# Kernel tuning notes

Hardware: AMD Instinct MI355X
Metric: run time of the kernel (lower is better)

The kernel has to match this reference:

```python
import jax, jax.numpy as jnp
import numpy as np

N_NODES = 50000
N_EDGES = 800000
N_FEAT = 128
HIDDEN = 128
N_CLASSES = 10
N_GRAPHS = 100


def setup_inputs() -> dict:
    key = jax.random.key(0)
    ks = jax.random.split(key, 16)
    x = jax.random.normal(ks[0], (N_NODES, N_FEAT), dtype=jnp.float32)
    edge_index = jax.random.randint(ks[1], (2, N_EDGES), 0, N_NODES, dtype=jnp.int64)
    batch = jnp.sort(jax.random.randint(ks[2], (N_NODES,), 0, N_GRAPHS, dtype=jnp.int64))

    def glorot(k, fi, fo):
        s = jnp.sqrt(6.0 / (fi + fo)).astype(jnp.float32)
        return jax.random.uniform(k, (fi, fo), jnp.float32, -s, s)

    return {
        "x": x,
        "edge_index": edge_index,
        "batch": batch,
        "W1": glorot(ks[3], N_FEAT, HIDDEN),
        "b1": jnp.zeros((HIDDEN,), jnp.float32),
        "W2": glorot(ks[4], HIDDEN, HIDDEN),
        "b2": jnp.zeros((HIDDEN,), jnp.float32),
        "W3": glorot(ks[5], HIDDEN, HIDDEN // 2),
        "b3": jnp.zeros((HIDDEN // 2,), jnp.float32),
        "Wf1": glorot(ks[6], HIDDEN // 2, 32),
        "bf1": jnp.zeros((32,), jnp.float32),
        "Wf2": glorot(ks[7], 32, N_CLASSES),
        "bf2": jnp.zeros((N_CLASSES,), jnp.float32),
    }


def _gcn_conv(x, row, col, norm, W, b, n_nodes):
    # GCNConv: x' = D^{-1/2}(A+I)D^{-1/2} (x W) + b
    h = x @ W                                            # [N, out]
    msg = h[row] * norm[:, None]                         # gather + scale per edge
    out = jax.ops.segment_sum(msg, col, num_segments=n_nodes)  # scatter-add to targets
    return out + b


def reference(x, edge_index, batch, W1, b1, W2, b2, W3, b3, Wf1, bf1, Wf2, bf2):
    n = x.shape[0]
    # add self-loops (PyG GCNConv default)
    loop = jnp.arange(n, dtype=edge_index.dtype)
    row = jnp.concatenate([edge_index[0], loop])
    col = jnp.concatenate([edge_index[1], loop])
    # symmetric normalization from in-degree at targets (edge_weight = 1)
    deg = jax.ops.segment_sum(jnp.ones_like(col, x.dtype), col, num_segments=n)
    dinv = jnp.where(deg > 0, jax.lax.rsqrt(deg), 0.0)
    norm = dinv[row] * dinv[col]                         # [E + N]

    h = jax.nn.relu(_gcn_conv(x, row, col, norm, W1, b1, n))
    h = jax.nn.relu(_gcn_conv(h, row, col, norm, W2, b2, n))
    h = jax.nn.relu(_gcn_conv(h, row, col, norm, W3, b3, n))

    # global_mean_pool over graphs
    sums = jax.ops.segment_sum(h, batch, num_segments=N_GRAPHS)
    cnts = jax.ops.segment_sum(jnp.ones((n,), h.dtype), batch, num_segments=N_GRAPHS)
    pooled = sums / jnp.maximum(cnts, 1.0)[:, None]      # [G, hidden//2]

    h = jax.nn.relu(pooled @ Wf1 + bf1)
    logits = h @ Wf2 + bf2                               # [G, num_classes]
    return logits
```

## Files before the change

### kernel.cpp

```cpp
#include <hip/hip_runtime.h>
#include <hip/hip_fp16.h>


#define NGRAPH 100
#define CAP 64

typedef _Float16 f16x8 __attribute__((ext_vector_type(8)));
typedef float f32x4 __attribute__((ext_vector_type(4)));
typedef float fx2 __attribute__((ext_vector_type(2)));
typedef float fx4 __attribute__((ext_vector_type(4)));


__global__ __launch_bounds__(256) void prep_all(const float* __restrict__ W1,
                                                const float* __restrict__ W2,
                                                const float* __restrict__ W3,
                                                __half* __restrict__ Wt1,
                                                __half* __restrict__ Wt2,
                                                __half* __restrict__ Wt3,
                                                int* __restrict__ cnt,
                                                float* __restrict__ pooled, int n) {
    const int idx = blockIdx.x * 256 + threadIdx.x;
    if (idx < 16384) {
        int nn = idx >> 7, k = idx & 127;
        Wt1[idx] = __float2half(W1[k * 128 + nn]);
    } else if (idx < 32768) {
        int j = idx - 16384;
        int nn = j >> 7, k = j & 127;
        Wt2[j] = __float2half(W2[k * 128 + nn]);
    } else if (idx < 40960) {
        int j = idx - 32768;
        int nn = j >> 7, k = j & 127;
        Wt3[j] = __float2half(W3[k * 64 + nn]);
    }
    if (idx < n) cnt[idx] = 0;
    if (idx < NGRAPH * 64) pooled[idx] = 0.0f;
}


__global__ void fill_bucket(const int* __restrict__ row, const int* __restrict__ col,
                            int* __restrict__ cnt, int* __restrict__ bucket,
                            int E, int colsPerGroup) {
    const int g  = blockIdx.x & 7;
    const int gb = blockIdx.x >> 3;
    const int nb = gridDim.x >> 3;
    const int lo = g * colsPerGroup, hi = lo + colsPerGroup;
    for (int e = gb * 256 + threadIdx.x; e < E; e += nb * 256) {
        int c = col[e];
        if (c >= lo && c < hi) {
            int pos = atomicAdd(&cnt[c], 1);
            bucket[c * CAP + pos] = row[e];
        }
    }
}


template <int OUT, bool F16IN>
__global__ __launch_bounds__(256) void gemm_mfma(const void* __restrict__ Xv,
                                                 const __half* __restrict__ Wt,
                                                 const float* __restrict__ bias_in,
                                                 const int* __restrict__ cnt,
                                                 __half* __restrict__ Yh, int n) {
    __shared__ _Float16 Xs[64 * 128];
    __shared__ _Float16 Ws[OUT * 128];
    __shared__ float bs[128];

    const float*  Xf = (const float*)Xv;
    const __half* Xh = (const __half*)Xv;

    const int t = threadIdx.x;
    if (t < 128) bs[t] = (bias_in != nullptr) ? bias_in[t] : 0.0f;
    __syncthreads();

    const int row0 = blockIdx.x * 64;
    const bool do_relu = (bias_in != nullptr);

    for (int c = t; c < 64 * 16; c += 256) {
        const int r = c >> 4, q = c & 15;
        const int gr = row0 + r;
        float vals[8];
        #pragma unroll
        for (int i = 0; i < 8; ++i) vals[i] = 0.0f;
        if (gr < n) {
            if (F16IN) {
                f16x8 hv = *(const f16x8*)&Xh[(size_t)gr * 128 + q * 8];
                #pragma unroll
                for (int i = 0; i < 8; ++i) vals[i] = (float)hv[i];
            } else {
                float4 va = *(const float4*)&Xf[(size_t)gr * 128 + q * 8];
                float4 vb = *(const float4*)&Xf[(size_t)gr * 128 + q * 8 + 4];
                vals[0] = va.x; vals[1] = va.y; vals[2] = va.z; vals[3] = va.w;
                vals[4] = vb.x; vals[5] = vb.y; vals[6] = vb.z; vals[7] = vb.w;
            }
        }
        if (do_relu) {
            const int k = q * 8;
            #pragma unroll
            for (int i = 0; i < 8; ++i) vals[i] = fmaxf(vals[i] + bs[k + i], 0.f);
        }
        f16x8 hv;
        #pragma unroll
        for (int i = 0; i < 8; ++i) hv[i] = (_Float16)vals[i];
        *(f16x8*)&Xs[(size_t)((r << 4) + (q ^ (r & 15))) * 8] = hv;
    }
    for (int c = t; c < OUT * 16; c += 256) {
        const int nn = c >> 4, q = c & 15;
        f16x8 w = *(const f16x8*)&Wt[nn * 128 + q * 8];
        *(f16x8*)&Ws[(size_t)((nn << 4) + (q ^ (nn & 15))) * 8] = w;
    }
    __syncthreads();

    constexpr int NT = OUT / 16;
    const int lane = t & 63, wave = t >> 6;
    const int m = lane & 15, quad = lane >> 4;

    f32x4 acc[NT];
    #pragma unroll
    for (int i = 0; i < NT; ++i) acc[i] = (f32x4){0.f, 0.f, 0.f, 0.f};

    #pragma unroll
    for (int s = 0; s < 4; ++s) {
        const int qa = s * 4 + quad;
        f16x8 a = *(const f16x8*)&Xs[(size_t)(((wave * 16 + m) << 4) + (qa ^ m)) * 8];
        #pragma unroll
        for (int tt = 0; tt < NT; ++tt) {
            f16x8 b = *(const f16x8*)&Ws[(size_t)(((tt * 16 + m) << 4) + (qa ^ m)) * 8];
            acc[tt] = __builtin_amdgcn_mfma_f32_16x16x32_f16(a, b, acc[tt], 0, 0, 0);
        }
    }

    #pragma unroll
    for (int i = 0; i < 4; ++i) {
        const int gr = row0 + wave * 16 + quad * 4 + i;
        if (gr < n) {
            const float dw = 1.0f / sqrtf((float)(cnt[gr] + 1));
            #pragma unroll
            for (int tt = 0; tt < NT; ++tt)
                Yh[(size_t)gr * OUT + tt * 16 + m] = __float2half(acc[tt][i] * dw);
        }
    }
}


template <int F>
__global__ void gather_kernel(const __half* __restrict__ hs, const int* __restrict__ cnt,
                              const int* __restrict__ bucket,
                              __half* __restrict__ outh, int n) {
    const int lane = threadIdx.x & 63;
    const int c = (blockIdx.x * blockDim.x + threadIdx.x) >> 6;
    if (c >= n) return;
    const int deg = cnt[c];
    const int beg = c * CAP;
    const int end = beg + deg;
    const int last = end - 1;
    const float w = 1.0f / sqrtf((float)(deg + 1));
    const float4* hq = (const float4*)hs;

    const int strm = lane >> 4;
    const int li   = lane & 15;

    float a[8];
    #pragma unroll
    for (int i = 0; i < 8; ++i) a[i] = 0.f;

    auto acc8 = [&](float4 raw, float m) {
        __half2 h0 = *(__half2*)&raw.x;
        __half2 h1 = *(__half2*)&raw.y;
        __half2 h2 = *(__half2*)&raw.z;
        __half2 h3 = *(__half2*)&raw.w;
        float2 f0 = __half22float2(h0), f1 = __half22float2(h1);
        float2 f2 = __half22float2(h2), f3 = __half22float2(h3);
        a[0] += m * f0.x; a[1] += m * f0.y;
        a[2] += m * f1.x; a[3] += m * f1.y;
        a[4] += m * f2.x; a[5] += m * f2.y;
        a[6] += m * f3.x; a[7] += m * f3.y;
    };

    if (strm == 0) acc8(hq[(size_t)c * 16 + li], 1.f);

    const int chunks = (deg + 15) >> 4;
    int j = beg + strm;
    for (int t = 0; t < chunks; ++t, j += 16) {
        const int j0 = j, j1 = j + 4, j2 = j + 8, j3 = j + 12;
        const int s0 = __builtin_nontemporal_load(&bucket[min(j0, last)]);
        const int s1 = __builtin_nontemporal_load(&bucket[min(j1, last)]);
        const int s2 = __builtin_nontemporal_load(&bucket[min(j2, last)]);
        const int s3 = __builtin_nontemporal_load(&bucket[min(j3, last)]);
        const float m0 = (j0 < end) ? 1.f : 0.f;
        const float m1 = (j1 < end) ? 1.f : 0.f;
        const float m2 = (j2 < end) ? 1.f : 0.f;
        const float m3 = (j3 < end) ? 1.f : 0.f;
        float4 v0 = hq[(size_t)s0 * 16 + li];
        float4 v1 = hq[(size_t)s1 * 16 + li];
        float4 v2 = hq[(size_t)s2 * 16 + li];
        float4 v3 = hq[(size_t)s3 * 16 + li];
        acc8(v0, m0);
        acc8(v1, m1);
        acc8(v2, m2);
        acc8(v3, m3);
    }

    #pragma unroll
    for (int i = 0; i < 8; ++i) {
        a[i] += __shfl(a[i], lane ^ 16);
        a[i] += __shfl(a[i], lane ^ 32);
    }
    if (strm == 0) {
        __half2 o0 = __float22half2_rn(make_float2(w * a[0], w * a[1]));
        __half2 o1 = __float22half2_rn(make_float2(w * a[2], w * a[3]));
        __half2 o2 = __float22half2_rn(make_float2(w * a[4], w * a[5]));
        __half2 o3 = __float22half2_rn(make_float2(w * a[6], w * a[7]));
        fx4 o;
        o[0] = *(float*)&o0;
        o[1] = *(float*)&o1;
        o[2] = *(float*)&o2;
        o[3] = *(float*)&o3;
        __builtin_nontemporal_store(o, (fx4*)&outh[(size_t)c * 128 + li * 8]);
    }
}


__global__ __launch_bounds__(256) void fused_gpool(const __half* __restrict__ hs,
                                                   const int* __restrict__ cnt,
                                                   const int* __restrict__ bucket,
                                                   const float* __restrict__ b3,
                                                   const int* __restrict__ batch,
                                                   float* __restrict__ pooled, int n) {
    const int lane  = threadIdx.x & 63;
    const int half  = lane >> 5;
    const int li    = lane & 31;
    const int wave  = (blockIdx.x * blockDim.x + threadIdx.x) >> 6;
    const int nwav  = (gridDim.x * blockDim.x) >> 6;
    const int chunk = (n + nwav - 1) / nwav;
    const int beg = wave * chunk;
    const int end = min(beg + chunk, n);
    if (beg >= end) return;
    const unsigned* h2 = (const unsigned*)hs;

    auto cvt2 = [](unsigned raw) { return __half22float2(*(__half2*)&raw); };

    const float bias0 = b3[li * 2], bias1 = b3[li * 2 + 1];
    int curg = batch[beg];
    float2 acc = make_float2(0.f, 0.f);
    for (int i = beg; i < end; ++i) {
        int g = batch[i];
        if (g != curg) {
            if (half == 0) {
                atomicAdd(&pooled[curg * 64 + li * 2],     acc.x);
                atomicAdd(&pooled[curg * 64 + li * 2 + 1], acc.y);
            }
            acc = make_float2(0.f, 0.f); curg = g;
        }
        const int deg = cnt[i];
        const float dv = 1.0f / sqrtf((float)(deg + 1));
        float2 sv = make_float2(0.f, 0.f);
        if (half == 0) sv = cvt2(h2[(size_t)i * 32 + li]);
        const int eb = i * CAP, ee = eb + deg;
        const int lastj = ee - 1;
        const int chks = (deg + 15) >> 4;
        int j = eb + half;
        for (int t = 0; t < chks; ++t, j += 16) {
            const int j0 = j,      j1 = j + 2,  j2 = j + 4,  j3 = j + 6;
            const int j4 = j + 8,  j5 = j + 10, j6 = j + 12, j7 = j + 14;
            const int a0 = __builtin_nontemporal_load(&bucket[min(j0, lastj)]);
            const int a1 = __builtin_nontemporal_load(&bucket[min(j1, lastj)]);
            const int a2 = __builtin_nontemporal_load(&bucket[min(j2, lastj)]);
            const int a3 = __builtin_nontemporal_load(&bucket[min(j3, lastj)]);
            const int a4 = __builtin_nontemporal_load(&bucket[min(j4, lastj)]);
            const int a5 = __builtin_nontemporal_load(&bucket[min(j5, lastj)]);
            const int a6 = __builtin_nontemporal_load(&bucket[min(j6, lastj)]);
            const int a7 = __builtin_nontemporal_load(&bucket[min(j7, lastj)]);
            const float m0 = (j0 < ee) ? 1.f : 0.f;
            const float m1 = (j1 < ee) ? 1.f : 0.f;
            const float m2 = (j2 < ee) ? 1.f : 0.f;
            const float m3 = (j3 < ee) ? 1.f : 0.f;
            const float m4 = (j4 < ee) ? 1.f : 0.f;
            const float m5 = (j5 < ee) ? 1.f : 0.f;
            const float m6 = (j6 < ee) ? 1.f : 0.f;
            const float m7 = (j7 < ee) ? 1.f : 0.f;
            float2 v0 = cvt2(h2[(size_t)a0 * 32 + li]);
            float2 v1 = cvt2(h2[(size_t)a1 * 32 + li]);
            float2 v2 = cvt2(h2[(size_t)a2 * 32 + li]);
            float2 v3 = cvt2(h2[(size_t)a3 * 32 + li]);
            float2 v4 = cvt2(h2[(size_t)a4 * 32 + li]);
            float2 v5 = cvt2(h2[(size_t)a5 * 32 + li]);
            float2 v6 = cvt2(h2[(size_t)a6 * 32 + li]);
            float2 v7 = cvt2(h2[(size_t)a7 * 32 + li]);
            sv.x += m0 * v0.x + m1 * v1.x + m2 * v2.x + m3 * v3.x
                  + m4 * v4.x + m5 * v5.x + m6 * v6.x + m7 * v7.x;
            sv.y += m0 * v0.y + m1 * v1.y + m2 * v2.y + m3 * v3.y
                  + m4 * v4.y + m5 * v5.y + m6 * v6.y + m7 * v7.y;
        }
        sv.x += __shfl(sv.x, lane ^ 32);
        sv.y += __shfl(sv.y, lane ^ 32);
        acc.x += fmaxf(dv * sv.x + bias0, 0.f);
        acc.y += fmaxf(dv * sv.y + bias1, 0.f);
    }
    if (half == 0) {
        atomicAdd(&pooled[curg * 64 + li * 2],     acc.x);
        atomicAdd(&pooled[curg * 64 + li * 2 + 1], acc.y);
    }
}


__global__ __launch_bounds__(64) void mlp_kernel(const float* __restrict__ pooled,
                                                 const int* __restrict__ batch,
                                                 const float* __restrict__ Wf1,
                                                 const float* __restrict__ bf1,
                                                 const float* __restrict__ Wf2,
                                                 const float* __restrict__ bf2,
                                                 float* __restrict__ out, int n) {
    const int g = blockIdx.x;
    const int t = threadIdx.x;

    auto lb = [&](int v) {
        int lo = 0, hi = n;
        while (lo < hi) { int mid = (lo + hi) >> 1; if (batch[mid] < v) lo = mid + 1; else hi = mid; }
        return lo;
    };
    const int cnt = lb(g + 1) - lb(g);

    __shared__ float pm[64];
    __shared__ float hid[32];

    pm[t] = pooled[g * 64 + t] / (float)(cnt > 0 ? cnt : 1);
    __syncthreads();

    if (t < 32) {
        float a = bf1[t];
        #pragma unroll
        for (int k = 0; k < 64; ++k) a += pm[k] * Wf1[k * 32 + t];
        hid[t] = fmaxf(a, 0.f);
    }
    __syncthreads();

    if (t < 10) {
        float a = bf2[t];
        #pragma unroll
        for (int k = 0; k < 32; ++k) a += hid[k] * Wf2[k * 10 + t];
        out[g * 10 + t] = a;
    }
}


extern "C" void kernel_launch(void* const* d_in, const int* in_sizes, int n_in,
                              void* d_out, int out_size, void* d_ws, size_t ws_size,
                              hipStream_t stream) {
    const float* x     = (const float*)d_in[0];
    const int*   edge  = (const int*)  d_in[1];
    const int*   batch = (const int*)  d_in[2];
    const float* W1    = (const float*)d_in[3];
    const float* b1    = (const float*)d_in[4];
    const float* W2    = (const float*)d_in[5];
    const float* b2    = (const float*)d_in[6];
    const float* W3    = (const float*)d_in[7];
    const float* b3    = (const float*)d_in[8];
    const float* Wf1   = (const float*)d_in[9];
    const float* bf1   = (const float*)d_in[10];
    const float* Wf2   = (const float*)d_in[11];
    const float* bf2   = (const float*)d_in[12];
    float* out = (float*)d_out;

    const int E = in_sizes[1] / 2;
    const int n = in_sizes[2];
    const int* row = edge;
    const int* col = edge + E;

    const int colsPerGroup = (n + 7) / 8;

    const size_t n_pad = ((size_t)n + 64) & ~(size_t)63;
    char* wsb = (char*)d_ws;
    int*    cnt    = (int*)wsb;                  wsb += n_pad * 4;
    float*  pooled = (float*)wsb;                wsb += NGRAPH * 64 * 4;
    int*    bucket = (int*)wsb;                  wsb += (size_t)n_pad * CAP * 4;
    __half* Wt1    = (__half*)wsb;               wsb += 16384 * 2;
    __half* Wt2    = (__half*)wsb;               wsb += 16384 * 2;
    __half* Wt3    = (__half*)wsb;               wsb += 8192 * 2;
    __half* bufA   = (__half*)wsb;               wsb += (size_t)n * 128 * 2;
    __half* bufB   = (__half*)wsb;

    prep_all<<<256, 256, 0, stream>>>(W1, W2, W3, Wt1, Wt2, Wt3, cnt, pooled, n);
    fill_bucket<<<1024, 256, 0, stream>>>(row, col, cnt, bucket, E, colsPerGroup);

    const int ggemm = (n + 63) / 64;
    const int gath_grid = (n * 64 + 255) / 256;

    gemm_mfma<128, false><<<ggemm, 256, 0, stream>>>(x, Wt1, nullptr, cnt, bufA, n);
    gather_kernel<128><<<gath_grid, 256, 0, stream>>>(bufA, cnt, bucket, bufB, n);
    gemm_mfma<128, true><<<ggemm, 256, 0, stream>>>(bufB, Wt2, b1, cnt, bufA, n);
    gather_kernel<128><<<gath_grid, 256, 0, stream>>>(bufA, cnt, bucket, bufB, n);
    gemm_mfma<64, true><<<ggemm, 256, 0, stream>>>(bufB, Wt3, b2, cnt, bufA, n);
    fused_gpool<<<2048, 256, 0, stream>>>(bufA, cnt, bucket, b3, batch, pooled, n);
    mlp_kernel<<<NGRAPH, 64, 0, stream>>>(pooled, batch, Wf1, bf1, Wf2, bf2, out, n);
}
```

Baseline: 263.5 us.

## Fuse neighbor gather with following layer GEMM via shared-memory tile

Replaces the separate gather kernel plus GEMM kernel for layers 2 and 3 with one kernel. Each block gathers and aggregates 64 destination rows, applies bias and ReLU, and stores the fp16 result in shared memory. It then runs the MFMA GEMM on that tile directly. This removes the intermediate global write and read of the aggregated features and one launch per layer. The cost is fewer waves in flight during the latency-bound gather phase: 782 blocks, each wave handling 16 rows in sequence, instead of one wave per row.

```diff
diff --git a/kernel.cpp b/kernel.cpp
--- a/kernel.cpp
+++ b/kernel.cpp
@@ -7,8 +7,6 @@
 
 typedef _Float16 f16x8 __attribute__((ext_vector_type(8)));
 typedef float f32x4 __attribute__((ext_vector_type(4)));
-typedef float fx2 __attribute__((ext_vector_type(2)));
-typedef float fx4 __attribute__((ext_vector_type(4)));
 
 
 __global__ __launch_bounds__(256) void prep_all(const float* __restrict__ W1,
@@ -141,80 +139,126 @@
 }
 
 
-template <int F>
-__global__ void gather_kernel(const __half* __restrict__ hs, const int* __restrict__ cnt,
-                              const int* __restrict__ bucket,
-                              __half* __restrict__ outh, int n) {
-    const int lane = threadIdx.x & 63;
-    const int c = (blockIdx.x * blockDim.x + threadIdx.x) >> 6;
-    if (c >= n) return;
-    const int deg = cnt[c];
-    const int beg = c * CAP;
-    const int end = beg + deg;
-    const int last = end - 1;
-    const float w = 1.0f / sqrtf((float)(deg + 1));
-    const float4* hq = (const float4*)hs;
-
+template <int OUT>
+__global__ __launch_bounds__(256) void gather_gemm(const __half* __restrict__ hs,
+                                                   const __half* __restrict__ Wt,
+                                                   const float* __restrict__ bias_in,
+                                                   const int* __restrict__ cnt,
+                                                   const int* __restrict__ bucket,
+                                                   __half* __restrict__ Yh, int n) {
+    __shared__ _Float16 Xs[64 * 128];
+    __shared__ _Float16 Ws[OUT * 128];
+    __shared__ float bs[128];
+
+    const int t = threadIdx.x;
+    if (t < 128) bs[t] = bias_in[t];
+
+    for (int c = t; c < OUT * 16; c += 256) {
+        const int nn = c >> 4, q = c & 15;
+        f16x8 w = *(const f16x8*)&Wt[nn * 128 + q * 8];
+        *(f16x8*)&Ws[(size_t)((nn << 4) + (q ^ (nn & 15))) * 8] = w;
+    }
+    __syncthreads();
+
+    const int row0 = blockIdx.x * 64;
+    const int wave = t >> 6, lane = t & 63;
     const int strm = lane >> 4;
     const int li   = lane & 15;
-
-    float a[8];
-    #pragma unroll
-    for (int i = 0; i < 8; ++i) a[i] = 0.f;
-
-    auto acc8 = [&](float4 raw, float m) {
-        __half2 h0 = *(__half2*)&raw.x;
-        __half2 h1 = *(__half2*)&raw.y;
-        __half2 h2 = *(__half2*)&raw.z;
-        __half2 h3 = *(__half2*)&raw.w;
-        float2 f0 = __half22float2(h0), f1 = __half22float2(h1);
-        float2 f2 = __half22float2(h2), f3 = __half22float2(h3);
-        a[0] += m * f0.x; a[1] += m * f0.y;
-        a[2] += m * f1.x; a[3] += m * f1.y;
-        a[4] += m * f2.x; a[5] += m * f2.y;
-        a[6] += m * f3.x; a[7] += m * f3.y;
-    };
-
-    if (strm == 0) acc8(hq[(size_t)c * 16 + li], 1.f);
-
-    const int chunks = (deg + 15) >> 4;
-    int j = beg + strm;
-    for (int t = 0; t < chunks; ++t, j += 16) {
-        const int j0 = j, j1 = j + 4, j2 = j + 8, j3 = j + 12;
-        const int s0 = __builtin_nontemporal_load(&bucket[min(j0, last)]);
-        const int s1 = __builtin_nontemporal_load(&bucket[min(j1, last)]);
-        const int s2 = __builtin_nontemporal_load(&bucket[min(j2, last)]);
-        const int s3 = __builtin_nontemporal_load(&bucket[min(j3, last)]);
-        const float m0 = (j0 < end) ? 1.f : 0.f;
-        const float m1 = (j1 < end) ? 1.f : 0.f;
-        const float m2 = (j2 < end) ? 1.f : 0.f;
-        const float m3 = (j3 < end) ? 1.f : 0.f;
-        float4 v0 = hq[(size_t)s0 * 16 + li];
-        float4 v1 = hq[(size_t)s1 * 16 + li];
-        float4 v2 = hq[(size_t)s2 * 16 + li];
-        float4 v3 = hq[(size_t)s3 * 16 + li];
-        acc8(v0, m0);
-        acc8(v1, m1);
-        acc8(v2, m2);
-        acc8(v3, m3);
-    }
-
-    #pragma unroll
-    for (int i = 0; i < 8; ++i) {
-        a[i] += __shfl(a[i], lane ^ 16);
-        a[i] += __shfl(a[i], lane ^ 32);
-    }
-    if (strm == 0) {
-        __half2 o0 = __float22half2_rn(make_float2(w * a[0], w * a[1]));
-        __half2 o1 = __float22half2_rn(make_float2(w * a[2], w * a[3]));
-        __half2 o2 = __float22half2_rn(make_float2(w * a[4], w * a[5]));
-        __half2 o3 = __float22half2_rn(make_float2(w * a[6], w * a[7]));
-        fx4 o;
-        o[0] = *(float*)&o0;
-        o[1] = *(float*)&o1;
-        o[2] = *(float*)&o2;
-        o[3] = *(float*)&o3;
-        __builtin_nontemporal_store(o, (fx4*)&outh[(size_t)c * 128 + li * 8]);
+    const float4* hq = (const float4*)hs;
+
+    for (int i = 0; i < 16; ++i) {
+        const int r = wave * 16 + i;
+        const int c = row0 + r;
+        float a[8];
+        #pragma unroll
+        for (int k = 0; k < 8; ++k) a[k] = 0.f;
+
+        auto acc8 = [&](float4 raw, float m) {
+            __half2 h0 = *(__half2*)&raw.x;
+            __half2 h1 = *(__half2*)&raw.y;
+            __half2 h2 = *(__half2*)&raw.z;
+            __half2 h3 = *(__half2*)&raw.w;
+            float2 f0 = __half22float2(h0), f1 = __half22float2(h1);
+            float2 f2 = __half22float2(h2), f3 = __half22float2(h3);
+            a[0] += m * f0.x; a[1] += m * f0.y;
+            a[2] += m * f1.x; a[3] += m * f1.y;
+            a[4] += m * f2.x; a[5] += m * f2.y;
+            a[6] += m * f3.x; a[7] += m * f3.y;
+        };
+
+        int deg = 0;
+        if (c < n) {
+            deg = cnt[c];
+            const int beg = c * CAP;
+            const int end = beg + deg;
+            const int last = end - 1;
+            if (strm == 0) acc8(hq[(size_t)c * 16 + li], 1.f);
+            const int chunks = (deg + 15) >> 4;
+            int j = beg + strm;
+            for (int tt = 0; tt < chunks; ++tt, j += 16) {
+                const int j0 = j, j1 = j + 4, j2 = j + 8, j3 = j + 12;
+                const int s0 = __builtin_nontemporal_load(&bucket[min(j0, last)]);
+                const int s1 = __builtin_nontemporal_load(&bucket[min(j1, last)]);
+                const int s2 = __builtin_nontemporal_load(&bucket[min(j2, last)]);
+                const int s3 = __builtin_nontemporal_load(&bucket[min(j3, last)]);
+                const float m0 = (j0 < end) ? 1.f : 0.f;
+                const float m1 = (j1 < end) ? 1.f : 0.f;
+                const float m2 = (j2 < end) ? 1.f : 0.f;
+                const float m3 = (j3 < end) ? 1.f : 0.f;
+                float4 v0 = hq[(size_t)s0 * 16 + li];
+                float4 v1 = hq[(size_t)s1 * 16 + li];
+                float4 v2 = hq[(size_t)s2 * 16 + li];
+                float4 v3 = hq[(size_t)s3 * 16 + li];
+                acc8(v0, m0);
+                acc8(v1, m1);
+                acc8(v2, m2);
+                acc8(v3, m3);
+            }
+        }
+        const float w = 1.0f / sqrtf((float)(deg + 1));
+
+        #pragma unroll
+        for (int k = 0; k < 8; ++k) {
+            a[k] += __shfl(a[k], lane ^ 16);
+            a[k] += __shfl(a[k], lane ^ 32);
+        }
+        if (strm == 0) {
+            f16x8 hv;
+            #pragma unroll
+            for (int k = 0; k < 8; ++k)
+                hv[k] = (_Float16)fmaxf(w * a[k] + bs[li * 8 + k], 0.f);
+            *(f16x8*)&Xs[(size_t)((r << 4) + (li ^ (r & 15))) * 8] = hv;
+        }
+    }
+    __syncthreads();
+
+    constexpr int NT = OUT / 16;
+    const int m = lane & 15, quad = lane >> 4;
+
+    f32x4 acc[NT];
+    #pragma unroll
+    for (int i = 0; i < NT; ++i) acc[i] = (f32x4){0.f, 0.f, 0.f, 0.f};
+
+    #pragma unroll
+    for (int s = 0; s < 4; ++s) {
+        const int qa = s * 4 + quad;
+        f16x8 av = *(const f16x8*)&Xs[(size_t)(((wave * 16 + m) << 4) + (qa ^ m)) * 8];
+        #pragma unroll
+        for (int tt = 0; tt < NT; ++tt) {
+            f16x8 bv = *(const f16x8*)&Ws[(size_t)(((tt * 16 + m) << 4) + (qa ^ m)) * 8];
+            acc[tt] = __builtin_amdgcn_mfma_f32_16x16x32_f16(av, bv, acc[tt], 0, 0, 0);
+        }
+    }
+
+    #pragma unroll
+    for (int i = 0; i < 4; ++i) {
+        const int gr = row0 + wave * 16 + quad * 4 + i;
+        if (gr < n) {
+            const float dw = 1.0f / sqrtf((float)(cnt[gr] + 1));
+            #pragma unroll
+            for (int tt = 0; tt < NT; ++tt)
+                Yh[(size_t)gr * OUT + tt * 16 + m] = __float2half(acc[tt][i] * dw);
+        }
     }
 }
 
@@ -382,13 +426,10 @@
     fill_bucket<<<1024, 256, 0, stream>>>(row, col, cnt, bucket, E, colsPerGroup);
 
     const int ggemm = (n + 63) / 64;
-    const int gath_grid = (n * 64 + 255) / 256;
 
     gemm_mfma<128, false><<<ggemm, 256, 0, stream>>>(x, Wt1, nullptr, cnt, bufA, n);
-    gather_kernel<128><<<gath_grid, 256, 0, stream>>>(bufA, cnt, bucket, bufB, n);
-    gemm_mfma<128, true><<<ggemm, 256, 0, stream>>>(bufB, Wt2, b1, cnt, bufA, n);
-    gather_kernel<128><<<gath_grid, 256, 0, stream>>>(bufA, cnt, bucket, bufB, n);
-    gemm_mfma<64, true><<<ggemm, 256, 0, stream>>>(bufB, Wt3, b2, cnt, bufA, n);
+    gather_gemm<128><<<ggemm, 256, 0, stream>>>(bufA, Wt2, b1, cnt, bucket, bufB, n);
+    gather_gemm<64><<<ggemm, 256, 0, stream>>>(bufB, Wt3, b2, cnt, bucket, bufA, n);
     fused_gpool<<<2048, 256, 0, stream>>>(bufA, cnt, bucket, b3, batch, pooled, n);
     mlp_kernel<<<NGRAPH, 64, 0, stream>>>(pooled, batch, Wf1, bf1, Wf2, bf2, out, n);
 }
```

Result: slower. 302.1 us (+14.6%).
